# Kernel optimization log

Hardware: AMD Instinct MI355X
Metric: run time of the kernel (lower is better)

The kernel has to match this reference:

```python
import jax
import jax.numpy as jnp
from jax import lax
import numpy as np

# ---- static RPN config (mirrors init_kwargs) ----
STRIDES = (8, 16)
SIZES = ((32, 32), (16, 16))
SCALES = ((64.0 ** 2,), (128.0 ** 2,))
RATIOS = ((0.5, 1.0, 2.0), (0.5, 1.0, 2.0))
IMAGE_SIZE = (256, 256)
NMS_THRESH = 0.7
POST_NMS_TOP_N = 2000
NUM_LEVELS = 2
TOP_K_PER_LEVEL = POST_NMS_TOP_N // NUM_LEVELS  # padded NMS output slots per level


def _generate_anchors(stride, scales, ratios, size, image_size):
    """Anchors of shape (H*W*A, 4) in (x1,y1,x2,y2), clamped to image."""
    H, W = size
    cy = (np.arange(H, dtype=np.float32) + 0.5) * stride
    cx = (np.arange(W, dtype=np.float32) + 0.5) * stride
    ws, hs = [], []
    for s in scales:
        for r in ratios:
            ws.append(np.sqrt(s / r))
            hs.append(np.sqrt(s * r))
    ws = np.asarray(ws, np.float32)  # [A]
    hs = np.asarray(hs, np.float32)
    cxg, cyg = np.meshgrid(cx, cy)  # [H, W]
    x1 = cxg[..., None] - 0.5 * ws
    y1 = cyg[..., None] - 0.5 * hs
    x2 = cxg[..., None] + 0.5 * ws
    y2 = cyg[..., None] + 0.5 * hs
    a = np.stack([x1, y1, x2, y2], axis=-1)  # [H, W, A, 4]
    a[..., 0] = np.clip(a[..., 0], 0, image_size[0])
    a[..., 1] = np.clip(a[..., 1], 0, image_size[1])
    a[..., 2] = np.clip(a[..., 2], 0, image_size[0])
    a[..., 3] = np.clip(a[..., 3], 0, image_size[1])
    return a.reshape(-1, 4).astype(np.float32)


ANCHORS = [
    _generate_anchors(STRIDES[i], SCALES[i], RATIOS[i], SIZES[i], IMAGE_SIZE)
    for i in range(NUM_LEVELS)
]


def conv2d(x, w, b, padding):
    y = lax.conv_general_dilated(
        x, w, window_strides=(1, 1), padding=padding,
        dimension_numbers=("NCHW", "OIHW", "NCHW"))
    return y + b[None, :, None, None]


def decode_boxes(anchors, deltas):
    """Standard R-CNN box decode. anchors [N,4], deltas [..., N, 4]."""
    wa = anchors[:, 2] - anchors[:, 0]
    ha = anchors[:, 3] - anchors[:, 1]
    cxa = anchors[:, 0] + 0.5 * wa
    cya = anchors[:, 1] + 0.5 * ha
    dx, dy, dw, dh = deltas[..., 0], deltas[..., 1], deltas[..., 2], deltas[..., 3]
    cx = dx * wa + cxa
    cy = dy * ha + cya
    w = jnp.exp(dw) * wa
    h = jnp.exp(dh) * ha
    return jnp.stack([cx - 0.5 * w, cy - 0.5 * h, cx + 0.5 * w, cy + 0.5 * h], axis=-1)


def clamp_boxes(b):
    return jnp.stack([
        jnp.clip(b[..., 0], 0.0, IMAGE_SIZE[0]),
        jnp.clip(b[..., 1], 0.0, IMAGE_SIZE[1]),
        jnp.clip(b[..., 2], 0.0, IMAGE_SIZE[0]),
        jnp.clip(b[..., 3], 0.0, IMAGE_SIZE[1]),
    ], axis=-1)


def _pairwise_iou(b):
    # b: [N, 4] -> [N, N] IoU (torchvision convention, no +1)
    area = (b[:, 2] - b[:, 0]) * (b[:, 3] - b[:, 1])
    lt = jnp.maximum(b[:, None, :2], b[None, :, :2])
    rb = jnp.minimum(b[:, None, 2:], b[None, :, 2:])
    wh = jnp.clip(rb - lt, 0.0)
    inter = wh[..., 0] * wh[..., 1]
    return inter / (area[:, None] + area[None, :] - inter)


def nms_padded(boxes, scores, thresh, top_k):
    """Exact greedy NMS; returns (top_k,4) boxes and (top_k,) scores padded with -1."""
    N = boxes.shape[0]
    order = jnp.argsort(-scores)
    b = boxes[order]
    s = scores[order]
    iou = _pairwise_iou(b)  # [N, N]

    def body(supp, xs):
        row, i = xs
        keep_i = jnp.logical_not(supp[i])
        supp = supp | (keep_i & (row > thresh) & (jnp.arange(N) > i))
        return supp, keep_i

    _, keep = lax.scan(body, jnp.zeros((N,), bool), (iou, jnp.arange(N)))
    rank = jnp.cumsum(keep) - 1  # position among kept, in score order
    slot = jnp.where(keep & (rank < top_k), rank, top_k)  # overflow -> dump row
    out_b = jnp.full((top_k + 1, 4), -1.0, boxes.dtype).at[slot].set(b)
    out_s = jnp.full((top_k + 1,), -1.0, scores.dtype).at[slot].set(s)
    return out_b[:top_k], out_s[:top_k]


def _rpn_level(feat, anchors, conv_w, conv_b, cls_w, cls_b, reg_w, reg_b):
    x = jax.nn.relu(conv2d(feat, conv_w, conv_b, "SAME"))
    cls = conv2d(x, cls_w, cls_b, "VALID")              # [BS, A, H, W]
    reg = conv2d(x, reg_w, reg_b, "VALID")              # [BS, 4A, H, W]
    BS, A, H, W = cls.shape
    cls = cls.transpose(0, 2, 3, 1).reshape(BS, -1)                      # [BS, HWA]
    reg = reg.transpose(0, 2, 3, 1).reshape(BS, H, W, A, 4).reshape(BS, -1, 4)
    boxes = clamp_boxes(decode_boxes(anchors, lax.stop_gradient(reg)))   # [BS, HWA, 4]
    scores = jax.nn.sigmoid(lax.stop_gradient(cls))                      # [BS, HWA]
    kb, ks = jax.vmap(lambda bb, ss: nms_padded(bb, ss, NMS_THRESH, TOP_K_PER_LEVEL))(boxes, scores)
    return kb, ks


def setup_inputs() -> dict:
    key = jax.random.key(0)
    ks = jax.random.split(key, 5)
    C = 256
    A = 3
    return {
        "feat0": jax.random.normal(ks[0], (4, C, 32, 32), jnp.float32),
        "feat1": jax.random.normal(ks[1], (4, C, 16, 16), jnp.float32),
        "conv_w": 0.01 * jax.random.normal(ks[2], (C, C, 3, 3), jnp.float32),
        "conv_b": jnp.zeros((C,), jnp.float32),
        "cls_w": 0.01 * jax.random.normal(ks[3], (A, C, 1, 1), jnp.float32),
        "cls_b": jnp.zeros((A,), jnp.float32),
        "reg_w": 0.01 * jax.random.normal(ks[4], (4 * A, C, 1, 1), jnp.float32),
        "reg_b": jnp.zeros((4 * A,), jnp.float32),
    }


def reference(feat0, feat1, conv_w, conv_b, cls_w, cls_b, reg_w, reg_b):
    feats = [feat0, feat1]
    kb_all, ks_all = [], []
    for i in range(NUM_LEVELS):
        kb, ks = _rpn_level(feats[i], jnp.asarray(ANCHORS[i]),
                            conv_w, conv_b, cls_w, cls_b, reg_w, reg_b)
        kb_all.append(kb)
        ks_all.append(ks)
    bboxes = jnp.concatenate(kb_all, axis=1)   # [BS, POST_NMS_TOP_N, 4]
    scores = jnp.concatenate(ks_all, axis=1)   # [BS, POST_NMS_TOP_N]
    idx = jnp.argsort(-scores, axis=1)         # descending; -1 pads go last
    bboxes = jnp.take_along_axis(bboxes, idx[..., None], axis=1)
    return bboxes
```

## Files before the change

### kernel.cpp

```cpp
#include <hip/hip_runtime.h>
#include <math.h>


__global__ __launch_bounds__(256, 4) void conv3_sk_u(
    const float* __restrict__ feat0, const float* __restrict__ feat1,
    const float* __restrict__ conv_w,
    double* __restrict__ part0, double* __restrict__ part1)
{
  __shared__ float Ald[2][16][64];
  __shared__ float Bld[2][16][64];
  const int t = threadIdx.x;
  const int bid = blockIdx.x;
  const float* feat;
  double* part;
  int oc_t, p_t, k_base, hw_sh, w_sh, H;
  if (bid < 1024) {
    int kc = bid >> 8;
    feat = feat0; part = part0 + (size_t)kc * 4096 * 256;
    oc_t = bid & 3; p_t = (bid >> 2) & 63;
    k_base = kc * 576; hw_sh = 10; w_sh = 5; H = 32;
  } else {
    int b2 = bid - 1024;
    int kc = b2 >> 6;
    feat = feat1; part = part1 + (size_t)kc * 1024 * 256;
    oc_t = b2 & 3; p_t = (b2 >> 2) & 15;
    k_base = kc * 576; hw_sh = 8; w_sh = 4; H = 16;
  }
  const int oc_base = oc_t * 64;
  const int p_base  = p_t * 64;
  const int wmask = H - 1, hwmask = (1 << hw_sh) - 1;
  const int skk = t >> 4;
  const int q4  = (t & 15) * 4;

  float a_r[4], b_r[4];
  auto load_tile = [&](int kt) {
    const int k0 = k_base + kt * 16;
    const float* wrow = conv_w + (size_t)(oc_base + q4) * 2304 + (k0 + skk);
#pragma unroll
    for (int u = 0; u < 4; ++u) a_r[u] = wrow[(size_t)u * 2304];
    int p = p_base + q4;
    int b = p >> hw_sh, pin = p & hwmask;
    int y = pin >> w_sh, x0 = pin & wmask;
    int k = k0 + skk;
    int ic = k / 9, rr = k - ic * 9;
    int ky = rr / 3, kx = rr - ky * 3;
    int iy = y + ky - 1;
    const float* frow = feat + (((b << 8) + ic) << hw_sh) + (iy << w_sh);
    bool yok = (unsigned)iy < (unsigned)H;
#pragma unroll
    for (int u = 0; u < 4; ++u) {
      int ix = x0 + u + kx - 1;
      b_r[u] = (yok && (unsigned)ix < (unsigned)H) ? frow[ix] : 0.f;
    }
  };

  const int ty4 = (t >> 4) * 4;
  const int tx4 = (t & 15) * 4;
  double acc[4][4] = {};

  load_tile(0);
  for (int kt = 0; kt < 36; ++kt) {
    const int buf = kt & 1;
    *(float4*)&Ald[buf][skk][q4] = make_float4(a_r[0], a_r[1], a_r[2], a_r[3]);
    *(float4*)&Bld[buf][skk][q4] = make_float4(b_r[0], b_r[1], b_r[2], b_r[3]);
    __syncthreads();
    if (kt + 1 < 36) load_tile(kt + 1);
#pragma unroll
    for (int kk = 0; kk < 16; ++kk) {
      float4 av = *(const float4*)&Ald[buf][kk][ty4];
      float4 bv = *(const float4*)&Bld[buf][kk][tx4];
      double ad[4] = {(double)av.x, (double)av.y, (double)av.z, (double)av.w};
      double bd[4] = {(double)bv.x, (double)bv.y, (double)bv.z, (double)bv.w};
#pragma unroll
      for (int i = 0; i < 4; ++i)
#pragma unroll
        for (int j = 0; j < 4; ++j) acc[i][j] += ad[i] * bd[j];
    }
  }
#pragma unroll
  for (int j = 0; j < 4; ++j) {
    int p = p_base + tx4 + j;
    double* row = part + (size_t)p * 256 + oc_base + ty4;
    *(double2*)&row[0] = make_double2(acc[0][j], acc[1][j]);
    *(double2*)&row[2] = make_double2(acc[2][j], acc[3][j]);
  }
}

__global__ __launch_bounds__(256) void rhd_k(
    const double* __restrict__ part0, const double* __restrict__ part1,
    const float* __restrict__ conv_b,
    const float* __restrict__ cls_w, const float* __restrict__ cls_b,
    const float* __restrict__ reg_w, const float* __restrict__ reg_b,
    float* __restrict__ box0, float* __restrict__ sc0,
    float* __restrict__ box1, float* __restrict__ sc1)
{
  int wid = (blockIdx.x * 256 + threadIdx.x) >> 6;
  int lane = threadIdx.x & 63;
  int lvl = wid >= 4096;
  const double* part = lvl ? part1 : part0;
  int p = lvl ? wid - 4096 : wid;
  int M = lvl ? 1024 : 4096;
  float xv[4];
#pragma unroll
  for (int q = 0; q < 4; ++q) {
    int c = lane + 64 * q;
    double s = (double)conv_b[c];
#pragma unroll
    for (int ks = 0; ks < 4; ++ks)
      s += part[(size_t)ks * M * 256 + (size_t)p * 256 + c];
    float f = (float)s;
    xv[q] = f > 0.f ? f : 0.f;
  }
  double acc[15];
#pragma unroll
  for (int o = 0; o < 15; ++o) {
    const float* wr = (o < 3) ? (cls_w + o * 256) : (reg_w + (o - 3) * 256);
    double a = 0.0;
#pragma unroll
    for (int q = 0; q < 4; ++q)
      a += (double)wr[lane + 64 * q] * (double)xv[q];
    acc[o] = a;
  }
#pragma unroll
  for (int d = 1; d < 64; d <<= 1)
#pragma unroll
    for (int o = 0; o < 15; ++o)
      acc[o] += __shfl_xor(acc[o], d, 64);
  if (lane < 3) {
    int a = lane;
    float cls = (float)(acc[a] + (double)cls_b[a]);
    float score = 1.f / (1.f + expf(-cls));
    float dx = (float)(acc[3 + a * 4 + 0] + (double)reg_b[a * 4 + 0]);
    float dy = (float)(acc[3 + a * 4 + 1] + (double)reg_b[a * 4 + 1]);
    float dw = (float)(acc[3 + a * 4 + 2] + (double)reg_b[a * 4 + 2]);
    float dh = (float)(acc[3 + a * 4 + 3] + (double)reg_b[a * 4 + 3]);
    int hw_sh = lvl ? 8 : 10, w_sh = lvl ? 4 : 5, Wd = lvl ? 16 : 32;
    float S = lvl ? 16.f : 8.f;
    double scale = lvl ? 16384.0 : 4096.0;
    int b = p >> hw_sh, pin = p & ((1 << hw_sh) - 1);
    int y = pin >> w_sh, x = pin & (Wd - 1);
    double ratio = (a == 0) ? 0.5 : (a == 1 ? 1.0 : 2.0);
    float w_a = (float)sqrt(scale / ratio);
    float h_a = (float)sqrt(scale * ratio);
    float cx = ((float)x + 0.5f) * S;
    float cy = ((float)y + 0.5f) * S;
    float x1 = cx - 0.5f * w_a, y1 = cy - 0.5f * h_a;
    float x2 = cx + 0.5f * w_a, y2 = cy + 0.5f * h_a;
    x1 = fminf(fmaxf(x1, 0.f), 256.f); y1 = fminf(fmaxf(y1, 0.f), 256.f);
    x2 = fminf(fmaxf(x2, 0.f), 256.f); y2 = fminf(fmaxf(y2, 0.f), 256.f);
    float wa = x2 - x1, ha = y2 - y1;
    float cxa = x1 + 0.5f * wa, cya = y1 + 0.5f * ha;
    float ncx = dx * wa + cxa;
    float ncy = dy * ha + cya;
    float nw = expf(dw) * wa;
    float nh = expf(dh) * ha;
    float bx1 = ncx - 0.5f * nw, by1 = ncy - 0.5f * nh;
    float bx2 = ncx + 0.5f * nw, by2 = ncy + 0.5f * nh;
    bx1 = fminf(fmaxf(bx1, 0.f), 256.f); by1 = fminf(fmaxf(by1, 0.f), 256.f);
    bx2 = fminf(fmaxf(bx2, 0.f), 256.f); by2 = fminf(fmaxf(by2, 0.f), 256.f);
    int n = pin * 3 + a;
    if (lvl) {
      ((float4*)box1)[(size_t)b * 768 + n] = make_float4(bx1, by1, bx2, by2);
      sc1[b * 768 + n] = score;
    } else {
      ((float4*)box0)[(size_t)b * 3072 + n] = make_float4(bx1, by1, bx2, by2);
      sc0[b * 3072 + n] = score;
    }
  }
}

__global__ __launch_bounds__(256) void sort_level_k(
    const float* __restrict__ sc0, const float* __restrict__ box0,
    float* __restrict__ ssc0, float* __restrict__ sbox0,
    const float* __restrict__ sc1, const float* __restrict__ box1,
    float* __restrict__ ssc1, float* __restrict__ sbox1)
{
  __shared__ float s[3072];
  int z = blockIdx.x;
  const float *sc, *box; float *ssc, *sbox; int N, b, c;
  if (z < 48) { sc = sc0; box = box0; ssc = ssc0; sbox = sbox0; N = 3072; b = z / 12; c = z % 12; }
  else { int z2 = z - 48; sc = sc1; box = box1; ssc = ssc1; sbox = sbox1; N = 768; b = z2 / 3; c = z2 % 3; }
  const float* scb = sc + (size_t)b * N;
  for (int j = threadIdx.x; j < N; j += 256) s[j] = scb[j];
  __syncthreads();
  int i = c * 256 + threadIdx.x;
  float si = s[i];
  int rank = 0;
  for (int j = 0; j < N; ++j) {
    float sj = s[j];
    rank += (sj > si) || (sj == si && j < i);
  }
  ssc[(size_t)b * N + rank] = si;
  float4 bi = ((const float4*)box)[(size_t)b * N + i];
  ((float4*)sbox)[(size_t)b * N + rank] = bi;
}

__global__ __launch_bounds__(256) void mask_col_k(
    const float* __restrict__ sbox0, const float* __restrict__ sbox1,
    unsigned long long* __restrict__ mask0, unsigned long long* __restrict__ mask1,
    unsigned long long* __restrict__ colD0, unsigned long long* __restrict__ colD1)
{
  int bid = blockIdx.x;
  if (bid < 2448) {
    __shared__ float4 bj[64];
    const float* sbox; unsigned long long* mask; int N, words, w, i_ch, b;
    if (bid < 2304) {
      sbox = sbox0; mask = mask0; N = 3072; words = 48;
      w = bid % 48; int r = bid / 48; i_ch = r % 12; b = r / 12;
    } else {
      int z = bid - 2304;
      sbox = sbox1; mask = mask1; N = 768; words = 12;
      w = z % 12; int r = z / 12; i_ch = r % 3; b = r / 3;
    }
    int i = i_ch * 256 + threadIdx.x;
    if (threadIdx.x < 64)
      bj[threadIdx.x] = ((const float4*)sbox)[(size_t)b * N + w * 64 + threadIdx.x];
    __syncthreads();
    float4 bi = ((const float4*)sbox)[(size_t)b * N + i];
    float ai = (bi.z - bi.x) * (bi.w - bi.y);
    unsigned long long m = 0ull;
#pragma unroll 16
    for (int jj = 0; jj < 64; ++jj) {
      int j = w * 64 + jj;
      float4 bv = bj[jj];
      float lx = fmaxf(bi.x, bv.x), ly = fmaxf(bi.y, bv.y);
      float rx = fminf(bi.z, bv.z), ry = fminf(bi.w, bv.w);
      float iw = fmaxf(rx - lx, 0.f), ih = fmaxf(ry - ly, 0.f);
      float inter = iw * ih;
      float aj = (bv.z - bv.x) * (bv.w - bv.y);
      float iou = inter / (ai + aj - inter);
      if ((iou > 0.7f) & (j > i)) m |= (1ull << jj);
    }
    mask[((size_t)b * N + i) * words + w] = m;
  } else {
    __shared__ float4 tb[4][64];
    int sub = threadIdx.x >> 6, lane = threadIdx.x & 63;
    const float* sbox; unsigned long long* colD; int N, tile, b;
    if (bid < 2496) {
      int unit = (bid - 2448) * 4 + sub;
      sbox = sbox0; colD = colD0; N = 3072;
      tile = unit % 48; b = unit / 48;
    } else {
      int unit = (bid - 2496) * 4 + sub;
      sbox = sbox1; colD = colD1; N = 768;
      tile = unit % 12; b = unit / 12;
    }
    tb[sub][lane] = ((const float4*)sbox)[(size_t)b * N + tile * 64 + lane];
    __syncthreads();
    float4 bq = tb[sub][lane];
    float aq = (bq.z - bq.x) * (bq.w - bq.y);
    unsigned long long col = 0ull;
#pragma unroll 16
    for (int ii = 0; ii < 64; ++ii) {
      float4 bi = tb[sub][ii];
      float lx = fmaxf(bq.x, bi.x), ly = fmaxf(bq.y, bi.y);
      float rx = fminf(bq.z, bi.z), ry = fminf(bq.w, bi.w);
      float iw = fmaxf(rx - lx, 0.f), ih = fmaxf(ry - ly, 0.f);
      float inter = iw * ih;
      float ai = (bi.z - bi.x) * (bi.w - bi.y);
      float iou = inter / (aq + ai - inter);
      if ((iou > 0.7f) & (lane > ii)) col |= (1ull << ii);
    }
    colD[(size_t)b * N + tile * 64 + lane] = col;
  }
}

__global__ __launch_bounds__(64) void nms_scan_k(
    const float* __restrict__ ssc0, const float* __restrict__ sbox0,
    const unsigned long long* __restrict__ mask0,
    const unsigned long long* __restrict__ colD0,
    const float* __restrict__ ssc1, const float* __restrict__ sbox1,
    const unsigned long long* __restrict__ mask1,
    const unsigned long long* __restrict__ colD1,
    float* __restrict__ cb, float* __restrict__ cs)
{
  int z = blockIdx.x;
  int lvl = z >> 2, b = z & 3;
  int N = lvl ? 768 : 3072;
  int words = lvl ? 12 : 48;
  const float* ssc = lvl ? ssc1 : ssc0;
  const float* sbox = lvl ? sbox1 : sbox0;
  const unsigned long long* mask = (lvl ? mask1 : mask0) + (size_t)b * N * words;
  const unsigned long long* colD = (lvl ? colD1 : colD0) + (size_t)b * N;
  const int lane = threadIdx.x;
  float* cbb = cb + ((size_t)b * 2000 + lvl * 1000) * 4;
  float* csb = cs + (size_t)b * 2000 + lvl * 1000;
  for (int q = lane; q < 1000; q += 64) {
    csb[q] = -1.f;
    ((float4*)cbb)[q] = make_float4(-1.f, -1.f, -1.f, -1.f);
  }
  unsigned long long removed = 0ull;
  int kept_base = 0;
  for (int t = 0; t < words; ++t) {
    unsigned long long wr = __shfl(removed, t);
    unsigned long long col = colD[t * 64 + lane];
    bool sup = (wr >> lane) & 1ull;
#pragma unroll
    for (int i = 0; i < 64; ++i) {
      unsigned long long supv = __ballot(sup);
      bool keep_i = !((supv >> i) & 1ull);
      sup = sup | (keep_i & ((col >> i) & 1ull));
    }
    unsigned long long keep64 = ~__ballot(sup);
    if (!sup) {
      int rank = kept_base + __popcll(keep64 & ((1ull << lane) - 1ull));
      if (rank < 1000) {
        int i = t * 64 + lane;
        csb[rank] = ssc[(size_t)b * N + i];
        ((float4*)cbb)[rank] = ((const float4*)sbox)[(size_t)b * N + i];
      }
    }
    if (lane > t && lane < words) {
      const unsigned long long* row = mask + (size_t)t * 64 * words + lane;
      unsigned long long acc = removed;
#pragma unroll 16
      for (int bb = 0; bb < 64; ++bb) {
        unsigned long long m = row[(size_t)bb * words];
        acc |= (((keep64 >> bb) & 1ull) ? m : 0ull);
      }
      removed = acc;
    }
    kept_base += __popcll(keep64);
  }
}

__global__ __launch_bounds__(256) void final_sort_k(
    const float* __restrict__ cs, const float* __restrict__ cb,
    float* __restrict__ out)
{
  __shared__ float s[2000];
  int b = blockIdx.x >> 3, c = blockIdx.x & 7;
  const float* csb = cs + (size_t)b * 2000;
  for (int j = threadIdx.x; j < 2000; j += 256) s[j] = csb[j];
  __syncthreads();
  if (threadIdx.x >= 250) return;
  int li = c * 250 + threadIdx.x;
  float si = s[li];
  int rank = 0;
  for (int j = 0; j < 2000; ++j) {
    float sj = s[j];
    rank += (sj > si) || (sj == si && j < li);
  }
  float4 bi = ((const float4*)cb)[(size_t)b * 2000 + li];
  ((float4*)out)[(size_t)b * 2000 + rank] = bi;
}

extern "C" void kernel_launch(void* const* d_in, const int* in_sizes, int n_in,
                              void* d_out, int out_size, void* d_ws, size_t ws_size,
                              hipStream_t stream) {
  const float* feat0  = (const float*)d_in[0];
  const float* feat1  = (const float*)d_in[1];
  const float* conv_w = (const float*)d_in[2];
  const float* conv_b = (const float*)d_in[3];
  const float* cls_w  = (const float*)d_in[4];
  const float* cls_b  = (const float*)d_in[5];
  const float* reg_w  = (const float*)d_in[6];
  const float* reg_b  = (const float*)d_in[7];

  char* p = (char*)d_ws;
  auto alloc = [&](size_t bytes) {
    char* r = p;
    p += (bytes + 255) & ~(size_t)255;
    return r;
  };
  double* part0 = (double*)alloc((size_t)4 * 4096 * 256 * 8);
  double* part1 = (double*)alloc((size_t)4 * 1024 * 256 * 8);
  float* box0 = (float*)alloc((size_t)4 * 3072 * 16);
  float* sc0  = (float*)alloc((size_t)4 * 3072 * 4);
  float* box1 = (float*)alloc((size_t)4 * 768 * 16);
  float* sc1  = (float*)alloc((size_t)4 * 768 * 4);
  float* sbox0 = (float*)alloc((size_t)4 * 3072 * 16);
  float* ssc0  = (float*)alloc((size_t)4 * 3072 * 4);
  float* sbox1 = (float*)alloc((size_t)4 * 768 * 16);
  float* ssc1  = (float*)alloc((size_t)4 * 768 * 4);
  unsigned long long* mask0 = (unsigned long long*)alloc((size_t)4 * 3072 * 48 * 8);
  unsigned long long* mask1 = (unsigned long long*)alloc((size_t)4 * 768 * 12 * 8);
  unsigned long long* colD0 = (unsigned long long*)alloc((size_t)4 * 3072 * 8);
  unsigned long long* colD1 = (unsigned long long*)alloc((size_t)4 * 768 * 8);
  float* cb = (float*)alloc((size_t)4 * 2000 * 16);
  float* cs = (float*)alloc((size_t)4 * 2000 * 4);

  conv3_sk_u<<<1280, 256, 0, stream>>>(feat0, feat1, conv_w, part0, part1);
  rhd_k<<<1280, 256, 0, stream>>>(part0, part1, conv_b, cls_w, cls_b,
                                  reg_w, reg_b, box0, sc0, box1, sc1);
  sort_level_k<<<60, 256, 0, stream>>>(sc0, box0, ssc0, sbox0,
                                       sc1, box1, ssc1, sbox1);
  mask_col_k<<<2508, 256, 0, stream>>>(sbox0, sbox1, mask0, mask1, colD0, colD1);
  nms_scan_k<<<8, 64, 0, stream>>>(ssc0, sbox0, mask0, colD0,
                                   ssc1, sbox1, mask1, colD1, cb, cs);
  final_sort_k<<<32, 256, 0, stream>>>(cs, cb, (float*)d_out);
}
```

Before: 564.4 us.

## Vectorize head and sort loads, prefetch NMS mask rows, stop scan early

The RPN head kernel now reads split-K partials, conv bias and cls/reg weights as double2/float4, giving each lane four contiguous channels. The rank-based sort kernels read shared-memory scores as float4 so each load feeds four comparisons. The NMS scan issues the mask-row loads before the serial ballot loop so their latency overlaps it. It also prefetches the next tile's column bits, scores and boxes, and exits once 1000 boxes are kept. The cost is more registers for the 32-entry prefetch buffer and a changed summation order in the head dot products.

```diff
diff --git a/kernel.cpp b/kernel.cpp
--- a/kernel.cpp
+++ b/kernel.cpp
@@ -100,26 +100,31 @@
   const double* part = lvl ? part1 : part0;
   int p = lvl ? wid - 4096 : wid;
   int M = lvl ? 1024 : 4096;
+  double s4[4];
+  {
+    float4 bv = ((const float4*)conv_b)[lane];
+    s4[0] = (double)bv.x; s4[1] = (double)bv.y;
+    s4[2] = (double)bv.z; s4[3] = (double)bv.w;
+  }
+#pragma unroll
+  for (int ks = 0; ks < 4; ++ks) {
+    const double2* pr = (const double2*)(part + (size_t)ks * M * 256 + (size_t)p * 256);
+    double2 a = pr[2 * lane], b = pr[2 * lane + 1];
+    s4[0] += a.x; s4[1] += a.y; s4[2] += b.x; s4[3] += b.y;
+  }
   float xv[4];
 #pragma unroll
   for (int q = 0; q < 4; ++q) {
-    int c = lane + 64 * q;
-    double s = (double)conv_b[c];
-#pragma unroll
-    for (int ks = 0; ks < 4; ++ks)
-      s += part[(size_t)ks * M * 256 + (size_t)p * 256 + c];
-    float f = (float)s;
+    float f = (float)s4[q];
     xv[q] = f > 0.f ? f : 0.f;
   }
   double acc[15];
 #pragma unroll
   for (int o = 0; o < 15; ++o) {
     const float* wr = (o < 3) ? (cls_w + o * 256) : (reg_w + (o - 3) * 256);
-    double a = 0.0;
-#pragma unroll
-    for (int q = 0; q < 4; ++q)
-      a += (double)wr[lane + 64 * q] * (double)xv[q];
-    acc[o] = a;
+    float4 wv = ((const float4*)wr)[lane];
+    acc[o] = (double)wv.x * (double)xv[0] + (double)wv.y * (double)xv[1] +
+             (double)wv.z * (double)xv[2] + (double)wv.w * (double)xv[3];
   }
 #pragma unroll
   for (int d = 1; d < 64; d <<= 1)
@@ -175,7 +180,7 @@
     const float* __restrict__ sc1, const float* __restrict__ box1,
     float* __restrict__ ssc1, float* __restrict__ sbox1)
 {
-  __shared__ float s[3072];
+  __shared__ __align__(16) float s[3072];
   int z = blockIdx.x;
   const float *sc, *box; float *ssc, *sbox; int N, b, c;
   if (z < 48) { sc = sc0; box = box0; ssc = ssc0; sbox = sbox0; N = 3072; b = z / 12; c = z % 12; }
@@ -186,9 +191,14 @@
   int i = c * 256 + threadIdx.x;
   float si = s[i];
   int rank = 0;
-  for (int j = 0; j < N; ++j) {
-    float sj = s[j];
-    rank += (sj > si) || (sj == si && j < i);
+  const float4* sv = (const float4*)s;
+  for (int j4 = 0; j4 < (N >> 2); ++j4) {
+    float4 v = sv[j4];
+    int j = j4 * 4;
+    rank += (v.x > si) || (v.x == si && (j + 0) < i);
+    rank += (v.y > si) || (v.y == si && (j + 1) < i);
+    rank += (v.z > si) || (v.z == si && (j + 2) < i);
+    rank += (v.w > si) || (v.w == si && (j + 3) < i);
   }
   ssc[(size_t)b * N + rank] = si;
   float4 bi = ((const float4*)box)[(size_t)b * N + i];
@@ -278,23 +288,33 @@
   int lvl = z >> 2, b = z & 3;
   int N = lvl ? 768 : 3072;
   int words = lvl ? 12 : 48;
-  const float* ssc = lvl ? ssc1 : ssc0;
-  const float* sbox = lvl ? sbox1 : sbox0;
+  const float* ssc = (lvl ? ssc1 : ssc0) + (size_t)b * N;
+  const float4* sbox = ((const float4*)(lvl ? sbox1 : sbox0)) + (size_t)b * N;
   const unsigned long long* mask = (lvl ? mask1 : mask0) + (size_t)b * N * words;
   const unsigned long long* colD = (lvl ? colD1 : colD0) + (size_t)b * N;
   const int lane = threadIdx.x;
-  float* cbb = cb + ((size_t)b * 2000 + lvl * 1000) * 4;
   float* csb = cs + (size_t)b * 2000 + lvl * 1000;
+  float4* cbb = (float4*)(cb + ((size_t)b * 2000 + lvl * 1000) * 4);
   for (int q = lane; q < 1000; q += 64) {
     csb[q] = -1.f;
-    ((float4*)cbb)[q] = make_float4(-1.f, -1.f, -1.f, -1.f);
+    cbb[q] = make_float4(-1.f, -1.f, -1.f, -1.f);
   }
   unsigned long long removed = 0ull;
   int kept_base = 0;
+  unsigned long long colv = colD[lane];
+  float sc_i = ssc[lane];
+  float4 bx_i = sbox[lane];
   for (int t = 0; t < words; ++t) {
     unsigned long long wr = __shfl(removed, t);
-    unsigned long long col = colD[t * 64 + lane];
+    bool doprop = (lane > t) && (lane < words);
+    const unsigned long long* row = mask + (size_t)t * 64 * words + lane;
+    unsigned long long v[32];
+    if (doprop) {
+#pragma unroll
+      for (int s = 0; s < 32; ++s) v[s] = row[(size_t)s * words];
+    }
     bool sup = (wr >> lane) & 1ull;
+    unsigned long long col = colv;
 #pragma unroll
     for (int i = 0; i < 64; ++i) {
       unsigned long long supv = __ballot(sup);
@@ -304,23 +324,27 @@
     unsigned long long keep64 = ~__ballot(sup);
     if (!sup) {
       int rank = kept_base + __popcll(keep64 & ((1ull << lane) - 1ull));
-      if (rank < 1000) {
-        int i = t * 64 + lane;
-        csb[rank] = ssc[(size_t)b * N + i];
-        ((float4*)cbb)[rank] = ((const float4*)sbox)[(size_t)b * N + i];
-      }
-    }
-    if (lane > t && lane < words) {
-      const unsigned long long* row = mask + (size_t)t * 64 * words + lane;
+      if (rank < 1000) { csb[rank] = sc_i; cbb[rank] = bx_i; }
+    }
+    kept_base += __popcll(keep64);
+    if (kept_base >= 1000) break;
+    if (t + 1 >= words) break;
+    {
+      int i2 = (t + 1) * 64 + lane;
+      colv = colD[i2]; sc_i = ssc[i2]; bx_i = sbox[i2];
+    }
+    if (doprop) {
       unsigned long long acc = removed;
-#pragma unroll 16
-      for (int bb = 0; bb < 64; ++bb) {
-        unsigned long long m = row[(size_t)bb * words];
-        acc |= (((keep64 >> bb) & 1ull) ? m : 0ull);
-      }
+#pragma unroll
+      for (int s = 0; s < 32; ++s)
+        acc |= (((keep64 >> s) & 1ull) ? v[s] : 0ull);
+#pragma unroll
+      for (int s = 0; s < 32; ++s) v[s] = row[(size_t)(32 + s) * words];
+#pragma unroll
+      for (int s = 0; s < 32; ++s)
+        acc |= (((keep64 >> (32 + s)) & 1ull) ? v[s] : 0ull);
       removed = acc;
     }
-    kept_base += __popcll(keep64);
   }
 }
 
@@ -328,7 +352,7 @@
     const float* __restrict__ cs, const float* __restrict__ cb,
     float* __restrict__ out)
 {
-  __shared__ float s[2000];
+  __shared__ __align__(16) float s[2000];
   int b = blockIdx.x >> 3, c = blockIdx.x & 7;
   const float* csb = cs + (size_t)b * 2000;
   for (int j = threadIdx.x; j < 2000; j += 256) s[j] = csb[j];
@@ -337,9 +361,14 @@
   int li = c * 250 + threadIdx.x;
   float si = s[li];
   int rank = 0;
-  for (int j = 0; j < 2000; ++j) {
-    float sj = s[j];
-    rank += (sj > si) || (sj == si && j < li);
+  const float4* sv = (const float4*)s;
+  for (int j4 = 0; j4 < 500; ++j4) {
+    float4 v = sv[j4];
+    int j = j4 * 4;
+    rank += (v.x > si) || (v.x == si && (j + 0) < li);
+    rank += (v.y > si) || (v.y == si && (j + 1) < li);
+    rank += (v.z > si) || (v.z == si && (j + 2) < li);
+    rank += (v.w > si) || (v.w == si && (j + 3) < li);
   }
   float4 bi = ((const float4*)cb)[(size_t)b * 2000 + li];
   ((float4*)out)[(size_t)b * 2000 + rank] = bi;
```

Measured after the change: 547.1 us. 1.03x faster.
